# Performance work log

Measured on AMD Instinct MI355X. Metric: run time of the kernel, lower is better.

Reference implementation:

```python
import jax, jax.numpy as jnp
import numpy as np

EPS = 1e-5

def group_norm(x, gamma, beta, groups):
    b, c, h, w = x.shape
    xg = x.reshape(b, groups, c // groups, h, w)
    mean = xg.mean(axis=(2, 3, 4), keepdims=True)
    var = xg.var(axis=(2, 3, 4), keepdims=True)
    xg = (xg - mean) * jax.lax.rsqrt(var + EPS)
    x = xg.reshape(b, c, h, w)
    return x * gamma[None, :, None, None] + beta[None, :, None, None]

def setup_inputs() -> dict:
    key = jax.random.key(0)
    ks = jax.random.split(key, 7)
    b, c, h, w = 8, 256, 64, 64
    x = jax.random.normal(ks[0], (b, c, h, w), dtype=jnp.float32)
    # GroupNorm affine params
    gamma = jnp.ones((c,), dtype=jnp.float32)
    beta = jnp.zeros((c,), dtype=jnp.float32)
    # 1x1 convs == linear maps over channel dim
    s = 1.0 / np.sqrt(c)
    w_qkv = jax.random.uniform(ks[1], (3 * c, c), jnp.float32, -s, s)
    b_qkv = jax.random.uniform(ks[2], (3 * c,), jnp.float32, -s, s)
    w_proj = jax.random.uniform(ks[3], (c, c), jnp.float32, -s, s)
    b_proj = jax.random.uniform(ks[4], (c,), jnp.float32, -s, s)
    return {"x": x, "gamma": gamma, "beta": beta, "w_qkv": w_qkv,
            "b_qkv": b_qkv, "w_proj": w_proj, "b_proj": b_proj}

def reference(x, gamma, beta, w_qkv, b_qkv, w_proj, b_proj):
    b, c, h, w = x.shape
    n = h * w
    h_in = x
    xn = group_norm(x, gamma, beta, groups=8)
    # 1x1 conv qkv: [b,c,h,w] -> [b,3c,h,w] -> [b,3c,n]
    qkv = jnp.einsum('oc,bchw->bohw', w_qkv, xn) + b_qkv[None, :, None, None]
    qkv = qkv.reshape(b, 3 * c, n)
    q, k, v = jnp.split(qkv, 3, axis=1)          # each [b,c,n]
    # attn = softmax(q^T k / sqrt(c)) over last dim
    scores = jnp.einsum('bci,bcj->bij', q, k) / jnp.sqrt(jnp.float32(c))
    attn = jax.nn.softmax(scores, axis=-1)       # [b,n,n]
    out = jnp.einsum('bij,bcj->bci', attn, v)    # [b,c,n]
    out = out.reshape(b, c, h, w)
    out = jnp.einsum('oc,bchw->bohw', w_proj, out) + b_proj[None, :, None, None]
    return h_in + out
```

## Files before the change

kernel.cpp:

```cpp
#include <hip/hip_runtime.h>
#include <hip/hip_bf16.h>
#include <stdint.h>

typedef __bf16 bf16_t;
typedef __bf16 bf16x8 __attribute__((ext_vector_type(8)));
typedef __bf16 bf16x4 __attribute__((ext_vector_type(4)));
typedef float f32x4 __attribute__((ext_vector_type(4)));
typedef float f32x16 __attribute__((ext_vector_type(16)));

#define NPIX 4096
#define CH 256

__global__ __launch_bounds__(256) void gn_partial_k(const float* __restrict__ x,
                                                    float* __restrict__ acc2) {
  int bg = blockIdx.x >> 3;
  int chunk = blockIdx.x & 7;
  const float4* xp = (const float4*)(x + (size_t)bg * 32 * NPIX) + chunk * (32 * NPIX / 4 / 8);
  float s = 0.f, ss = 0.f;
  for (int i = threadIdx.x; i < 32 * NPIX / 4 / 8; i += 256) {
    float4 v = xp[i];
    s  += v.x + v.y + v.z + v.w;
    ss += v.x * v.x + v.y * v.y + v.z * v.z + v.w * v.w;
  }
  int l = threadIdx.x & 63, w = threadIdx.x >> 6;
  #pragma unroll
  for (int off = 32; off; off >>= 1) { s += __shfl_down(s, off); ss += __shfl_down(ss, off); }
  __shared__ float rs[4], rss[4];
  if (l == 0) { rs[w] = s; rss[w] = ss; }
  __syncthreads();
  if (threadIdx.x == 0) {
    atomicAdd(&acc2[bg * 2],     rs[0] + rs[1] + rs[2] + rs[3]);
    atomicAdd(&acc2[bg * 2 + 1], rss[0] + rss[1] + rss[2] + rss[3]);
  }
}

__global__ void gn_finalize_k(const float* __restrict__ acc2, float* __restrict__ stats) {
  int bg = threadIdx.x;
  float mean = acc2[bg * 2] * (1.f / (32.f * NPIX));
  float var  = acc2[bg * 2 + 1] * (1.f / (32.f * NPIX)) - mean * mean;
  stats[bg * 2]     = mean;
  stats[bg * 2 + 1] = rsqrtf(var + 1e-5f);
}

__global__ __launch_bounds__(256) void gn_apply_t_k(const float* __restrict__ x,
    const float* __restrict__ stats, const float* __restrict__ gamma,
    const float* __restrict__ beta, bf16_t* __restrict__ xnT) {
  __shared__ float tile[32][33];
  int b = blockIdx.z;
  int p0 = blockIdx.x * 32, c0 = blockIdx.y * 32;
  int g = c0 >> 5;
  float mean = stats[(b * 8 + g) * 2], rstd = stats[(b * 8 + g) * 2 + 1];
  int tx = threadIdx.x, ty = threadIdx.y;
  const float* xb = x + ((size_t)b * CH + c0) * NPIX + p0;
  #pragma unroll
  for (int j = 0; j < 4; ++j) {
    int c = ty + j * 8;
    float v = xb[(size_t)c * NPIX + tx];
    tile[c][tx] = (v - mean) * rstd * gamma[c0 + c] + beta[c0 + c];
  }
  __syncthreads();
  bf16_t* op = xnT + ((size_t)b * NPIX + p0) * CH + c0;
  #pragma unroll
  for (int j = 0; j < 4; ++j) {
    int p = ty + j * 8;
    op[(size_t)p * CH + tx] = (bf16_t)tile[tx][p];
  }
}

__global__ __launch_bounds__(256) void cast_w_k(const float* __restrict__ wq,
    const float* __restrict__ wp, bf16_t* __restrict__ wqb, bf16_t* __restrict__ wpb) {
  int i = blockIdx.x * 256 + threadIdx.x;
  if (i < 768 * 256) wqb[i] = (bf16_t)wq[i];
  if (i < 256 * 256) wpb[i] = (bf16_t)wp[i];
}

#define LSTR 80

template <int MODE>
__global__ __launch_bounds__(256) void gemm_nt_k(
    const bf16_t* __restrict__ Ag, const bf16_t* __restrict__ Bg,
    int lda, int ldb, int K,
    void* __restrict__ O0, void* __restrict__ O1,
    const float* __restrict__ bias, const float* __restrict__ resid) {
  __shared__ __align__(16) char ldsA[128 * LSTR];
  __shared__ __align__(16) char ldsB[128 * LSTR];

  const int t = threadIdx.x;
  const int l = t & 63;
  const int w = t >> 6;
  const int wr = w >> 1, wc = w & 1;
  const int bm = blockIdx.x * 128;
  const int bn = blockIdx.y * 128;
  const int bz = blockIdx.z;

  const bf16_t* Ap = Ag;
  const bf16_t* Bp = Bg;
  if constexpr (MODE == 0) Ap += (size_t)bz * NPIX * CH;
  if constexpr (MODE == 3) Bp += (size_t)bz * NPIX * CH;

  f32x4 acc[4][4] = {};

  const int srow = t >> 2;
  const int scol = (t & 3) * 8;

  for (int k0 = 0; k0 < K; k0 += 32) {
    __syncthreads();
    #pragma unroll
    for (int it = 0; it < 2; ++it) {
      int r = it * 64 + srow;
      *(bf16x8*)(ldsA + r * LSTR + scol * 2) =
          *(const bf16x8*)(Ap + (size_t)(bm + r) * lda + k0 + scol);
      *(bf16x8*)(ldsB + r * LSTR + scol * 2) =
          *(const bf16x8*)(Bp + (size_t)(bn + r) * ldb + k0 + scol);
    }
    __syncthreads();
    bf16x8 fa[4], fb[4];
    #pragma unroll
    for (int m = 0; m < 4; ++m)
      fa[m] = *(const bf16x8*)(ldsA + (wr * 64 + m * 16 + (l & 15)) * LSTR + (l >> 4) * 16);
    #pragma unroll
    for (int n = 0; n < 4; ++n)
      fb[n] = *(const bf16x8*)(ldsB + (wc * 64 + n * 16 + (l & 15)) * LSTR + (l >> 4) * 16);
    #pragma unroll
    for (int m = 0; m < 4; ++m)
      #pragma unroll
      for (int n = 0; n < 4; ++n)
        acc[m][n] = __builtin_amdgcn_mfma_f32_16x16x32_bf16(fa[m], fb[n], acc[m][n], 0, 0, 0);
  }

  const int r0 = bm + wr * 64 + (l >> 4) * 4;
  const int c0 = bn + wc * 64 + (l & 15);
  #pragma unroll
  for (int m = 0; m < 4; ++m) {
    #pragma unroll
    for (int n = 0; n < 4; ++n) {
      int col = c0 + n * 16;
      #pragma unroll
      for (int j = 0; j < 4; ++j) {
        int row = r0 + m * 16 + j;
        float v = acc[m][n][j];
        if constexpr (MODE == 0) {
          float val = v + bias[col];
          if (col < 256) val *= 0.09016844006f;
          if (col < 512)
            ((bf16_t*)O0)[(size_t)bz * NPIX * 512 + (size_t)row * 512 + col] = (bf16_t)val;
          else
            ((bf16_t*)O1)[(size_t)bz * CH * NPIX + (size_t)(col - 512) * NPIX + row] = (bf16_t)val;
        } else {
          size_t idx = (size_t)bz * CH * NPIX + (size_t)row * NPIX + col;
          ((float*)O0)[idx] = v + bias[row] + resid[idx];
        }
      }
    }
  }
}

#define KVB 64
#define KBYTES 32768
#define VBYTES 32768

__device__ __forceinline__ void dma16(const void* g, void* l) {
  __builtin_amdgcn_global_load_lds(
      (const __attribute__((address_space(1))) unsigned int*)g,
      (__attribute__((address_space(3))) unsigned int*)l, 16, 0, 0);
}

__device__ inline unsigned int pack2bf(float lo, float hi) {
  unsigned short a = __builtin_bit_cast(unsigned short, (bf16_t)lo);
  unsigned short b = __builtin_bit_cast(unsigned short, (bf16_t)hi);
  return (unsigned int)a | ((unsigned int)b << 16);
}

__global__ __launch_bounds__(512, 2) void flash_k(
    const bf16_t* __restrict__ qkT, const bf16_t* __restrict__ vglob,
    bf16_t* __restrict__ OT) {
  __shared__ __align__(16) char kS[2 * KBYTES];
  __shared__ __align__(16) char vS[2 * VBYTES];
  __shared__ float mls[8][2][32];

  const int t = threadIdx.x;
  const int l = t & 63, w = t >> 6;
  const int lq = l & 31, h = l >> 5;
  const int g = w >> 1, half = w & 1;
  const int batch = blockIdx.x & 7;
  const int q0 = (blockIdx.x >> 3) * 128;

  const bf16_t* qk_b = qkT + (size_t)batch * NPIX * 512;
  const bf16_t* v_b  = vglob + (size_t)batch * CH * NPIX;

  bf16x8 qf[16];
  const bf16_t* qrow = qk_b + (size_t)(q0 + g * 32 + lq) * 512 + h * 8;
  #pragma unroll
  for (int kk = 0; kk < 16; ++kk) qf[kk] = *(const bf16x8*)(qrow + kk * 16);

  const int krow_l = w * 8 + (l >> 5);
  const int kslot  = l & 31;
  const int vrow_l = w * 32 + (l >> 3);
  const int vslot  = l & 7;
  const bf16_t* ksrc = qk_b + 256;

  auto stage = [&](int tile, int buf) {
    #pragma unroll
    for (int it = 0; it < 4; ++it) {
      int r = krow_l + it * 2;
      dma16(ksrc + (size_t)(tile * KVB + r) * 512 + ((kslot ^ (r & 31)) << 3),
            kS + buf * KBYTES + (w * 8 + it * 2) * 512);
      int c = vrow_l + it * 8;
      dma16(v_b + (size_t)c * NPIX + tile * KVB + ((vslot ^ (c & 7)) << 3),
            vS + buf * VBYTES + (w * 32 + it * 8) * 128);
    }
  };

  stage(0, 0);
  __syncthreads();

  f32x16 acc_o[8] = {};
  float m = -1e30f, lsum = 0.f;
  const int krow = half * 32 + lq;
  const char* kbase = kS + krow * 512;
  const int kxor = (h << 4) ^ (lq << 4);
  const int vxor = (half << 6) ^ (h << 4) ^ ((lq & 7) << 4);
  const char* vlane = vS + lq * 128;

  for (int tile = 0; tile < 64; ++tile) {
    const int cur = tile & 1;
    if (tile < 63) stage(tile + 1, cur ^ 1);

    f32x16 s = {};
    const char* kb = kbase + cur * KBYTES;
    __builtin_amdgcn_s_setprio(1);
    #pragma unroll
    for (int kk = 0; kk < 16; ++kk) {
      bf16x8 kf = *(const bf16x8*)(kb + (kxor ^ (kk << 5)));
      s = __builtin_amdgcn_mfma_f32_32x32x16_bf16(kf, qf[kk], s, 0, 0, 0);
    }
    __builtin_amdgcn_s_setprio(0);

    float m0 = fmaxf(s[0], s[1]),   m1 = fmaxf(s[2], s[3]);
    float m2 = fmaxf(s[4], s[5]),   m3 = fmaxf(s[6], s[7]);
    float m4 = fmaxf(s[8], s[9]),   m5 = fmaxf(s[10], s[11]);
    float m6 = fmaxf(s[12], s[13]), m7 = fmaxf(s[14], s[15]);
    m0 = fmaxf(m0, m1); m2 = fmaxf(m2, m3); m4 = fmaxf(m4, m5); m6 = fmaxf(m6, m7);
    float tmax = fmaxf(fmaxf(m0, m2), fmaxf(m4, m6));
    tmax = fmaxf(tmax, __shfl_xor(tmax, 32, 64));
    if (!__all(tmax <= m + 10.f)) {
      float mnew = fmaxf(m, tmax);
      float sc = exp2f(m - mnew);
      m = mnew; lsum *= sc;
      #pragma unroll
      for (int n2 = 0; n2 < 8; ++n2)
        #pragma unroll
        for (int r = 0; r < 16; ++r) acc_o[n2][r] *= sc;
    }
    #pragma unroll
    for (int r = 0; r < 16; ++r) s[r] = exp2f(s[r] - m);
    float a0 = s[0] + s[1],   a1 = s[2] + s[3];
    float a2 = s[4] + s[5],   a3 = s[6] + s[7];
    float a4 = s[8] + s[9],   a5 = s[10] + s[11];
    float a6 = s[12] + s[13], a7 = s[14] + s[15];
    a0 += a1; a2 += a3; a4 += a5; a6 += a7;
    float ls = (a0 + a2) + (a4 + a6);
    ls += __shfl_xor(ls, 32, 64);
    lsum += ls;

    bf16x8 pa[2];
    #pragma unroll
    for (int kk2 = 0; kk2 < 2; ++kk2) {
      const int hi = kk2 * 8;
      unsigned int wkeep[2], wsend[2];
      #pragma unroll
      for (int j = 0; j < 2; ++j) {
        float b0 = s[2 * j + hi],     c0 = s[2 * j + 1 + hi];
        float b1 = s[2 * j + 4 + hi], c1v = s[2 * j + 5 + hi];
        float ka = h ? b1 : b0, kb2 = h ? c1v : c0;
        float sa = h ? b0 : b1, sb = h ? c0 : c1v;
        wkeep[j] = pack2bf(ka, kb2);
        wsend[j] = pack2bf(sa, sb);
      }
      unsigned int wr0 = __shfl_xor(wsend[0], 32, 64);
      unsigned int wr1 = __shfl_xor(wsend[1], 32, 64);
      union { unsigned int u[4]; bf16x8 v; } pu;
      pu.u[0] = h ? wr0 : wkeep[0];
      pu.u[1] = h ? wr1 : wkeep[1];
      pu.u[2] = h ? wkeep[0] : wr0;
      pu.u[3] = h ? wkeep[1] : wr1;
      pa[kk2] = pu.v;
    }

    const char* vb = vlane + cur * VBYTES;
    __builtin_amdgcn_s_setprio(1);
    #pragma unroll
    for (int n2 = 0; n2 < 8; ++n2) {
      const char* vp = vb + n2 * 4096;
      #pragma unroll
      for (int kk2 = 0; kk2 < 2; ++kk2) {
        bf16x8 vf = *(const bf16x8*)(vp + (vxor ^ (kk2 << 5)));
        acc_o[n2] = __builtin_amdgcn_mfma_f32_32x32x16_bf16(pa[kk2], vf, acc_o[n2], 0, 0, 0);
      }
    }
    __builtin_amdgcn_s_setprio(0);
    __syncthreads();
  }

  if (h == 0) { mls[w][0][lq] = m; mls[w][1][lq] = lsum; }
  char* abuf = (g < 2) ? (kS + g * 32768) : (vS + (g - 2) * 32768);
  if (half == 1) {
    float* ab = (float*)abuf + l * 128;
    #pragma unroll
    for (int n2 = 0; n2 < 8; ++n2)
      #pragma unroll
      for (int q4 = 0; q4 < 4; ++q4) {
        f32x4 vv;
        vv[0] = acc_o[n2][q4 * 4 + 0]; vv[1] = acc_o[n2][q4 * 4 + 1];
        vv[2] = acc_o[n2][q4 * 4 + 2]; vv[3] = acc_o[n2][q4 * 4 + 3];
        *(f32x4*)(ab + n2 * 16 + q4 * 4) = vv;
      }
  }
  __syncthreads();
  if (half == 0) {
    float mB = mls[w + 1][0][lq], lB = mls[w + 1][1][lq];
    float mS = fmaxf(m, mB);
    float sA = exp2f(m - mS), sB = exp2f(mB - mS);
    float inv = 1.f / (lsum * sA + lB * sB);
    const float* ab = (const float*)abuf + l * 128;
    bf16_t* obase = OT + (size_t)batch * NPIX * CH + (size_t)(q0 + g * 32) * CH + lq;
    #pragma unroll
    for (int r = 0; r < 16; ++r) {
      int q = (r & 3) + 8 * (r >> 2) + 4 * h;
      float sAr = __shfl(sA, q, 64);
      float sBr = __shfl(sB, q, 64);
      float ivr = __shfl(inv, q, 64);
      bf16_t* orow = obase + (size_t)q * CH;
      #pragma unroll
      for (int n2 = 0; n2 < 8; ++n2) {
        float ob = (acc_o[n2][r] * sAr + ab[n2 * 16 + r] * sBr) * ivr;
        orow[n2 * 32] = (bf16_t)ob;
      }
    }
  }
}

extern "C" void kernel_launch(void* const* d_in, const int* in_sizes, int n_in,
                              void* d_out, int out_size, void* d_ws, size_t ws_size,
                              hipStream_t stream) {
  const float* x      = (const float*)d_in[0];
  const float* gamma  = (const float*)d_in[1];
  const float* beta   = (const float*)d_in[2];
  const float* w_qkv  = (const float*)d_in[3];
  const float* b_qkv  = (const float*)d_in[4];
  const float* w_proj = (const float*)d_in[5];
  const float* b_proj = (const float*)d_in[6];

  char* p = (char*)d_ws;
  auto alloc = [&](size_t bytes) {
    char* r = p;
    p += (bytes + 255) & ~(size_t)255;
    return (void*)r;
  };
  bf16_t* qkT  = (bf16_t*)alloc((size_t)8 * NPIX * 512 * 2);
  bf16_t* vbuf = (bf16_t*)alloc((size_t)8 * CH * NPIX * 2);
  bf16_t* OT   = (bf16_t*)alloc((size_t)8 * NPIX * CH * 2);
  bf16_t* wqb  = (bf16_t*)alloc(768 * 256 * 2);
  bf16_t* wpb  = (bf16_t*)alloc(256 * 256 * 2);
  float*  acc2 = (float*)alloc(64 * 2 * 4);
  float*  stats= (float*)alloc(64 * 2 * 4);
  bf16_t* xnT  = (bf16_t*)d_out;

  hipMemsetAsync(acc2, 0, 64 * 2 * 4, stream);
  gn_partial_k<<<64 * 8, 256, 0, stream>>>(x, acc2);
  gn_finalize_k<<<1, 64, 0, stream>>>(acc2, stats);
  gn_apply_t_k<<<dim3(128, 8, 8), dim3(32, 8), 0, stream>>>(x, stats, gamma, beta, xnT);
  cast_w_k<<<768, 256, 0, stream>>>(w_qkv, w_proj, wqb, wpb);

  gemm_nt_k<0><<<dim3(32, 6, 8), 256, 0, stream>>>(xnT, wqb, CH, CH, CH,
                                                   qkT, vbuf, b_qkv, nullptr);
  flash_k<<<256, 512, 0, stream>>>(qkT, vbuf, OT);

  gemm_nt_k<3><<<dim3(2, 32, 8), 256, 0, stream>>>(wpb, OT, CH, CH, CH,
                                                   d_out, nullptr, b_proj, x);
}
```

Baseline: 362.1 us.

## Switch attention Q/K/V and probabilities to FP8 MFMA with smaller blocks

The QKV GEMM epilogue now writes Q, K and V as FP8 (e4m3) instead of bf16. The flash attention kernel uses fp8 32x32x16 MFMAs for both QK^T and PV, halving LDS tiles and global traffic, with reworked swizzles and a simpler P repack. Blocks shrink to 256 threads and 64 queries each, with the grid doubled. The rescale threshold is tightened to 8, and FP8 precision risks larger numerical error in scores and probabilities.

```diff
diff --git a/kernel.cpp b/kernel.cpp
--- a/kernel.cpp
+++ b/kernel.cpp
@@ -4,7 +4,6 @@
 
 typedef __bf16 bf16_t;
 typedef __bf16 bf16x8 __attribute__((ext_vector_type(8)));
-typedef __bf16 bf16x4 __attribute__((ext_vector_type(4)));
 typedef float f32x4 __attribute__((ext_vector_type(4)));
 typedef float f32x16 __attribute__((ext_vector_type(16)));
 
@@ -74,6 +73,10 @@
   if (i < 256 * 256) wpb[i] = (bf16_t)wp[i];
 }
 
+__device__ __forceinline__ unsigned char to_fp8(float v) {
+  return (unsigned char)(__builtin_amdgcn_cvt_pk_fp8_f32(v, 0.f, 0, 0) & 0xff);
+}
+
 #define LSTR 80
 
 template <int MODE>
@@ -143,9 +146,9 @@
           float val = v + bias[col];
           if (col < 256) val *= 0.09016844006f;
           if (col < 512)
-            ((bf16_t*)O0)[(size_t)bz * NPIX * 512 + (size_t)row * 512 + col] = (bf16_t)val;
+            ((unsigned char*)O0)[(size_t)bz * NPIX * 512 + (size_t)row * 512 + col] = to_fp8(val);
           else
-            ((bf16_t*)O1)[(size_t)bz * CH * NPIX + (size_t)(col - 512) * NPIX + row] = (bf16_t)val;
+            ((unsigned char*)O1)[(size_t)bz * CH * NPIX + (size_t)(col - 512) * NPIX + row] = to_fp8(val);
         } else {
           size_t idx = (size_t)bz * CH * NPIX + (size_t)row * NPIX + col;
           ((float*)O0)[idx] = v + bias[row] + resid[idx];
@@ -156,8 +159,8 @@
 }
 
 #define KVB 64
-#define KBYTES 32768
-#define VBYTES 32768
+#define KB8 16384
+#define VB8 16384
 
 __device__ __forceinline__ void dma16(const void* g, void* l) {
   __builtin_amdgcn_global_load_lds(
@@ -165,49 +168,49 @@
       (__attribute__((address_space(3))) unsigned int*)l, 16, 0, 0);
 }
 
-__device__ inline unsigned int pack2bf(float lo, float hi) {
-  unsigned short a = __builtin_bit_cast(unsigned short, (bf16_t)lo);
-  unsigned short b = __builtin_bit_cast(unsigned short, (bf16_t)hi);
-  return (unsigned int)a | ((unsigned int)b << 16);
-}
-
-__global__ __launch_bounds__(512, 2) void flash_k(
-    const bf16_t* __restrict__ qkT, const bf16_t* __restrict__ vglob,
+__device__ __forceinline__ unsigned int pk4(float a, float b, float c, float d) {
+  int r = __builtin_amdgcn_cvt_pk_fp8_f32(a, b, 0, 0);
+  r = __builtin_amdgcn_cvt_pk_fp8_f32(c, d, r, 1);
+  return (unsigned int)r;
+}
+
+__global__ __launch_bounds__(256, 2) void flash_k(
+    const unsigned char* __restrict__ qkT, const unsigned char* __restrict__ vglob,
     bf16_t* __restrict__ OT) {
-  __shared__ __align__(16) char kS[2 * KBYTES];
-  __shared__ __align__(16) char vS[2 * VBYTES];
-  __shared__ float mls[8][2][32];
+  __shared__ __align__(16) char kS[2 * KB8];
+  __shared__ __align__(16) char vS[2 * VB8];
+  __shared__ float mls[4][2][32];
 
   const int t = threadIdx.x;
   const int l = t & 63, w = t >> 6;
   const int lq = l & 31, h = l >> 5;
   const int g = w >> 1, half = w & 1;
   const int batch = blockIdx.x & 7;
-  const int q0 = (blockIdx.x >> 3) * 128;
-
-  const bf16_t* qk_b = qkT + (size_t)batch * NPIX * 512;
-  const bf16_t* v_b  = vglob + (size_t)batch * CH * NPIX;
-
-  bf16x8 qf[16];
-  const bf16_t* qrow = qk_b + (size_t)(q0 + g * 32 + lq) * 512 + h * 8;
-  #pragma unroll
-  for (int kk = 0; kk < 16; ++kk) qf[kk] = *(const bf16x8*)(qrow + kk * 16);
-
-  const int krow_l = w * 8 + (l >> 5);
-  const int kslot  = l & 31;
-  const int vrow_l = w * 32 + (l >> 3);
-  const int vslot  = l & 7;
-  const bf16_t* ksrc = qk_b + 256;
+  const int q0 = (blockIdx.x >> 3) * 64;
+
+  const unsigned char* qk_b = qkT + (size_t)batch * NPIX * 512;
+  const unsigned char* v_b  = vglob + (size_t)batch * CH * NPIX;
+
+  unsigned long qf[16];
+  const unsigned char* qrow = qk_b + (size_t)(q0 + g * 32 + lq) * 512 + h * 8;
+  #pragma unroll
+  for (int kk = 0; kk < 16; ++kk) qf[kk] = *(const unsigned long*)(qrow + kk * 16);
+
+  const int kRowL = t >> 4;
+  const int kChunk0 = (t & 15) ^ (t >> 4);
+  const int vRowL = t >> 2;
+  const int vChunk = ((t & 3) ^ ((t >> 3) & 3)) << 4;
+  const unsigned char* ksrc = qk_b + 256;
 
   auto stage = [&](int tile, int buf) {
     #pragma unroll
     for (int it = 0; it < 4; ++it) {
-      int r = krow_l + it * 2;
-      dma16(ksrc + (size_t)(tile * KVB + r) * 512 + ((kslot ^ (r & 31)) << 3),
-            kS + buf * KBYTES + (w * 8 + it * 2) * 512);
-      int c = vrow_l + it * 8;
-      dma16(v_b + (size_t)c * NPIX + tile * KVB + ((vslot ^ (c & 7)) << 3),
-            vS + buf * VBYTES + (w * 32 + it * 8) * 128);
+      int kr = it * 16 + kRowL;
+      dma16(ksrc + (size_t)(tile * KVB + kr) * 512 + ((kChunk0 ^ ((it & 1) << 3)) << 4),
+            kS + buf * KB8 + it * 4096 + w * 1024);
+      int vr = it * 64 + vRowL;
+      dma16(v_b + (size_t)vr * NPIX + tile * KVB + vChunk,
+            vS + buf * VB8 + it * 4096 + w * 1024);
     }
   };
 
@@ -217,22 +220,22 @@
   f32x16 acc_o[8] = {};
   float m = -1e30f, lsum = 0.f;
   const int krow = half * 32 + lq;
-  const char* kbase = kS + krow * 512;
-  const int kxor = (h << 4) ^ (lq << 4);
-  const int vxor = (half << 6) ^ (h << 4) ^ ((lq & 7) << 4);
-  const char* vlane = vS + lq * 128;
+  const char* kbase = kS + krow * 256;
+  const int koff = (h << 3) | (((lq & 15) ^ ((lq >> 4) << 3)) << 4);
+  const int vxor = (h << 3) | ((((half << 1) ^ ((lq >> 1) & 3))) << 4);
+  const char* vlane = vS + lq * 64;
 
   for (int tile = 0; tile < 64; ++tile) {
     const int cur = tile & 1;
     if (tile < 63) stage(tile + 1, cur ^ 1);
 
     f32x16 s = {};
-    const char* kb = kbase + cur * KBYTES;
+    const char* kb = kbase + cur * KB8;
     __builtin_amdgcn_s_setprio(1);
     #pragma unroll
     for (int kk = 0; kk < 16; ++kk) {
-      bf16x8 kf = *(const bf16x8*)(kb + (kxor ^ (kk << 5)));
-      s = __builtin_amdgcn_mfma_f32_32x32x16_bf16(kf, qf[kk], s, 0, 0, 0);
+      long kf = *(const long*)(kb + (koff ^ (kk << 4)));
+      s = __builtin_amdgcn_mfma_f32_32x32x16_fp8_fp8(kf, (long)qf[kk], s, 0, 0, 0);
     }
     __builtin_amdgcn_s_setprio(0);
 
@@ -243,7 +246,7 @@
     m0 = fmaxf(m0, m1); m2 = fmaxf(m2, m3); m4 = fmaxf(m4, m5); m6 = fmaxf(m6, m7);
     float tmax = fmaxf(fmaxf(m0, m2), fmaxf(m4, m6));
     tmax = fmaxf(tmax, __shfl_xor(tmax, 32, 64));
-    if (!__all(tmax <= m + 10.f)) {
+    if (!__all(tmax <= m + 8.f)) {
       float mnew = fmaxf(m, tmax);
       float sc = exp2f(m - mnew);
       m = mnew; lsum *= sc;
@@ -263,39 +266,29 @@
     ls += __shfl_xor(ls, 32, 64);
     lsum += ls;
 
-    bf16x8 pa[2];
+    unsigned long pa[2];
     #pragma unroll
     for (int kk2 = 0; kk2 < 2; ++kk2) {
       const int hi = kk2 * 8;
-      unsigned int wkeep[2], wsend[2];
-      #pragma unroll
-      for (int j = 0; j < 2; ++j) {
-        float b0 = s[2 * j + hi],     c0 = s[2 * j + 1 + hi];
-        float b1 = s[2 * j + 4 + hi], c1v = s[2 * j + 5 + hi];
-        float ka = h ? b1 : b0, kb2 = h ? c1v : c0;
-        float sa = h ? b0 : b1, sb = h ? c0 : c1v;
-        wkeep[j] = pack2bf(ka, kb2);
-        wsend[j] = pack2bf(sa, sb);
-      }
-      unsigned int wr0 = __shfl_xor(wsend[0], 32, 64);
-      unsigned int wr1 = __shfl_xor(wsend[1], 32, 64);
-      union { unsigned int u[4]; bf16x8 v; } pu;
-      pu.u[0] = h ? wr0 : wkeep[0];
-      pu.u[1] = h ? wr1 : wkeep[1];
-      pu.u[2] = h ? wkeep[0] : wr0;
-      pu.u[3] = h ? wkeep[1] : wr1;
-      pa[kk2] = pu.v;
-    }
-
-    const char* vb = vlane + cur * VBYTES;
+      unsigned int own_lo = pk4(s[hi + 0], s[hi + 1], s[hi + 2], s[hi + 3]);
+      unsigned int own_hi = pk4(s[hi + 4], s[hi + 5], s[hi + 6], s[hi + 7]);
+      unsigned int keep = h ? own_hi : own_lo;
+      unsigned int send = h ? own_lo : own_hi;
+      unsigned int recv = __shfl_xor(send, 32, 64);
+      unsigned int lo32 = h ? recv : keep;
+      unsigned int hi32 = h ? keep : recv;
+      pa[kk2] = ((unsigned long)hi32 << 32) | lo32;
+    }
+
+    const char* vb = vlane + cur * VB8;
     __builtin_amdgcn_s_setprio(1);
     #pragma unroll
     for (int n2 = 0; n2 < 8; ++n2) {
-      const char* vp = vb + n2 * 4096;
+      const char* vp = vb + n2 * 2048;
       #pragma unroll
       for (int kk2 = 0; kk2 < 2; ++kk2) {
-        bf16x8 vf = *(const bf16x8*)(vp + (vxor ^ (kk2 << 5)));
-        acc_o[n2] = __builtin_amdgcn_mfma_f32_32x32x16_bf16(pa[kk2], vf, acc_o[n2], 0, 0, 0);
+        long vf = *(const long*)(vp + (vxor ^ (kk2 << 4)));
+        acc_o[n2] = __builtin_amdgcn_mfma_f32_32x32x16_fp8_fp8((long)pa[kk2], vf, acc_o[n2], 0, 0, 0);
       }
     }
     __builtin_amdgcn_s_setprio(0);
@@ -303,7 +296,7 @@
   }
 
   if (h == 0) { mls[w][0][lq] = m; mls[w][1][lq] = lsum; }
-  char* abuf = (g < 2) ? (kS + g * 32768) : (vS + (g - 2) * 32768);
+  char* abuf = g == 0 ? kS : vS;
   if (half == 1) {
     float* ab = (float*)abuf + l * 128;
     #pragma unroll
@@ -357,8 +350,8 @@
     p += (bytes + 255) & ~(size_t)255;
     return (void*)r;
   };
-  bf16_t* qkT  = (bf16_t*)alloc((size_t)8 * NPIX * 512 * 2);
-  bf16_t* vbuf = (bf16_t*)alloc((size_t)8 * CH * NPIX * 2);
+  unsigned char* qkT  = (unsigned char*)alloc((size_t)8 * NPIX * 512);
+  unsigned char* vbuf = (unsigned char*)alloc((size_t)8 * CH * NPIX);
   bf16_t* OT   = (bf16_t*)alloc((size_t)8 * NPIX * CH * 2);
   bf16_t* wqb  = (bf16_t*)alloc(768 * 256 * 2);
   bf16_t* wpb  = (bf16_t*)alloc(256 * 256 * 2);
@@ -374,7 +367,7 @@
 
   gemm_nt_k<0><<<dim3(32, 6, 8), 256, 0, stream>>>(xnT, wqb, CH, CH, CH,
                                                    qkT, vbuf, b_qkv, nullptr);
-  flash_k<<<256, 512, 0, stream>>>(qkT, vbuf, OT);
+  flash_k<<<512, 256, 0, stream>>>(qkT, vbuf, OT);
 
   gemm_nt_k<3><<<dim3(2, 32, 8), 256, 0, stream>>>(wpb, OT, CH, CH, CH,
                                                    d_out, nullptr, b_proj, x);
```

After: 313.5 us. 1.15x faster.
